# Kernel tuning notes

Hardware: AMD Instinct MI355X
Metric: run time of the kernel (lower is better)

## Reference

```python
import jax, jax.numpy as jnp
import numpy as np

N_NODES = 100000
N_EDGES = 640000
NODE_DIM = 128
EDGE_DIM = 128


def setup_inputs() -> dict:
    key = jax.random.key(0)
    ks = jax.random.split(key, 12)
    sc_n = 1.0 / np.sqrt(NODE_DIM).astype(np.float32)
    sc_e = 1.0 / np.sqrt(EDGE_DIM).astype(np.float32)
    sc_c = 1.0 / np.sqrt(2 * EDGE_DIM).astype(np.float32)
    return {
        "V": jax.random.normal(ks[0], (N_NODES, NODE_DIM), jnp.float32),
        "E": jax.random.normal(ks[1], (N_EDGES, EDGE_DIM), jnp.float32),
        "src": jax.random.randint(ks[2], (N_EDGES,), 0, N_NODES),
        "dst": jax.random.randint(ks[3], (N_EDGES,), 0, N_NODES),
        "U_w": jax.random.normal(ks[4], (EDGE_DIM, NODE_DIM), jnp.float32) * sc_n,
        "V_w": jax.random.normal(ks[5], (EDGE_DIM, NODE_DIM), jnp.float32) * sc_n,
        "P_w": jax.random.normal(ks[6], (EDGE_DIM, EDGE_DIM), jnp.float32) * sc_e,
        "P_b": jax.random.normal(ks[7], (EDGE_DIM,), jnp.float32) * sc_e,
        "W1": jax.random.normal(ks[8], (EDGE_DIM, 2 * EDGE_DIM), jnp.float32) * sc_c,
        "b1": jax.random.normal(ks[9], (EDGE_DIM,), jnp.float32) * sc_c,
        "W2": jax.random.normal(ks[10], (EDGE_DIM, EDGE_DIM), jnp.float32) * sc_e,
        "b2": jax.random.normal(ks[11], (EDGE_DIM,), jnp.float32) * sc_e,
    }


def reference(V, E, src, dst, U_w, V_w, P_w, P_b, W1, b1, W2, b2):
    # E = LeakyReLU(E)  (torch default negative_slope = 0.01)
    E_a = jax.nn.leaky_relu(E, negative_slope=0.01)  # [n_edges, edge_dim]
    # EdgePooling: P(tanh(U(V[src]) * V(V[dst])))
    h_src = jnp.einsum("en,dn->ed", V[src], U_w)      # gather + project
    h_dst = jnp.einsum("en,dn->ed", V[dst], V_w)
    pooled = jnp.tanh(h_src * h_dst) @ P_w.T + P_b    # [n_edges, edge_dim]
    # concat with edge data, then MLP (Linear+ReLU per layer)
    h = jnp.concatenate([pooled, E_a], axis=-1)       # [n_edges, 2*edge_dim]
    h = jax.nn.relu(h @ W1.T + b1)
    h = jax.nn.relu(h @ W2.T + b2)
    return h
```

## Files before the change

kernel.cpp:

```cpp
#include <hip/hip_runtime.h>

typedef __attribute__((ext_vector_type(8))) short short8;
typedef __attribute__((ext_vector_type(4))) short short4v;
typedef __attribute__((ext_vector_type(4))) float float4v;

#define N_EDGES 640000

__device__ __forceinline__ short f2bf(float f) {
  union { float f; unsigned u; } a; a.f = f;
  unsigned r = a.u + 0x7FFFu + ((a.u >> 16) & 1u);
  return (short)(r >> 16);
}

__device__ __forceinline__ float fast_tanh(float x) {
  float xc = fminf(fmaxf(x, -15.f), 15.f);
  float e = __expf(2.f * xc);
  return (e - 1.f) * __builtin_amdgcn_rcpf(e + 1.f);
}


__global__ void prep_cvt(const float* __restrict__ U_w, const float* __restrict__ V_w,
                         const float* __restrict__ W1, const float* __restrict__ W2,
                         short* __restrict__ ws) {
  int i = blockIdx.x * 256 + threadIdx.x;
  if (i < 16384) {
    ws[i] = f2bf(U_w[i]);
  } else if (i < 32768) {
    ws[i] = f2bf(V_w[i - 16384]);
  } else if (i < 49152) {
    int j = i - 32768;
    ws[i + 16384] = f2bf(W1[(j >> 7) * 256 + 128 + (j & 127)]);
  } else {
    int j = i - 49152;
    ws[i + 16384] = f2bf(W2[j]);
  }
}

__global__ void prep_mm(const float* __restrict__ W1, const float* __restrict__ P_w,
                        const float* __restrict__ P_b, const float* __restrict__ b1,
                        short* __restrict__ ws) {
  int i = blockIdx.x * 256 + threadIdx.x;
  int o = i >> 7, k = i & 127;
  const float* wrow = W1 + o * 256;
  const float* pcol = P_w + k;
  float a0 = 0.f, a1 = 0.f, a2 = 0.f, a3 = 0.f;
#pragma unroll
  for (int c = 0; c < 128; c += 4) {
    a0 += wrow[c]     * pcol[c * 128];
    a1 += wrow[c + 1] * pcol[(c + 1) * 128];
    a2 += wrow[c + 2] * pcol[(c + 2) * 128];
    a3 += wrow[c + 3] * pcol[(c + 3) * 128];
  }
  ws[32768 + i] = f2bf((a0 + a1) + (a2 + a3));
  if (i < 128) {
    const float* wr = W1 + i * 256;
    float b = b1[i];
    for (int c = 0; c < 128; c++) b += wr[c] * P_b[c];
    ((float*)(ws + 81920))[i] = b;
  }
}

__global__ __launch_bounds__(256, 4) void fused_kernel(
    const float* __restrict__ V, const float* __restrict__ E,
    const int* __restrict__ src, const int* __restrict__ dst,
    const short* __restrict__ wbf,
    const float* __restrict__ b2, float* __restrict__ out) {
  __shared__ short bufA[64][136];
  __shared__ short bufB[64][136];

  const int tid  = threadIdx.x;
  const int lane = tid & 63;
  const int wave = tid >> 6;
  const int l15  = lane & 15;
  const int quad = lane >> 4;
  const int eb   = blockIdx.x * 64;
  const int n0   = wave * 2;

  const short* wU   = wbf;
  const short* wV   = wbf + 16384;
  const short* wM1  = wbf + 32768;
  const short* wW1b = wbf + 49152;
  const short* wW2  = wbf + 65536;
  const float* b1p  = (const float*)(wbf + 81920);

  float b1v[2], b2v[2];
#pragma unroll
  for (int n = 0; n < 2; n++) {
    int c = (n0 + n) * 16 + l15;
    b1v[n] = b1p[c]; b2v[n] = b2[c];
  }

  for (int i = tid; i < 2048; i += 256) {
    int row = i >> 5;
    int ch  = i & 31;
    int e   = eb + row;
    int s = src[e], d = dst[e];
    float4v vs = *((const float4v*)(V + (size_t)s * 128) + ch);
    float4v vd = *((const float4v*)(V + (size_t)d * 128) + ch);
    short4v ps = {f2bf(vs[0]), f2bf(vs[1]), f2bf(vs[2]), f2bf(vs[3])};
    short4v pd = {f2bf(vd[0]), f2bf(vd[1]), f2bf(vd[2]), f2bf(vd[3])};
    *(short4v*)&bufA[row][ch * 4] = ps;
    *(short4v*)&bufB[row][ch * 4] = pd;
  }
  __syncthreads();

  short8 tpk[4];
  float4v ef[8];
#pragma unroll
  for (int m = 0; m < 4; m++) {
    float4v accS[2] = {(float4v){0.f,0.f,0.f,0.f}, (float4v){0.f,0.f,0.f,0.f}};
    float4v accD[2] = {(float4v){0.f,0.f,0.f,0.f}, (float4v){0.f,0.f,0.f,0.f}};
#pragma unroll
    for (int kk = 0; kk < 4; kk++) {
      short8 bU[2], bV[2];
#pragma unroll
      for (int n = 0; n < 2; n++) {
        const int off = ((n0 + n) * 16 + l15) * 128 + kk * 32 + quad * 8;
        bU[n] = *(const short8*)(wU + off);
        bV[n] = *(const short8*)(wV + off);
      }
      short8 aS = *(const short8*)&bufA[m * 16 + l15][kk * 32 + quad * 8];
      short8 aD = *(const short8*)&bufB[m * 16 + l15][kk * 32 + quad * 8];
#pragma unroll
      for (int n = 0; n < 2; n++) {
        accS[n] = __builtin_amdgcn_mfma_f32_16x16x32_bf16(aS, bU[n], accS[n], 0, 0, 0);
        accD[n] = __builtin_amdgcn_mfma_f32_16x16x32_bf16(aD, bV[n], accD[n], 0, 0, 0);
      }
    }
    if (m == 2) {
#pragma unroll
      for (int i = 0; i < 8; i++) {
        int idx = tid + (i << 8);
        int row = idx >> 5;
        int ch  = idx & 31;
        ef[i] = __builtin_nontemporal_load(
            (const float4v*)(E + (size_t)(eb + row) * 128) + ch);
      }
    }
    short tv[8];
#pragma unroll
    for (int n = 0; n < 2; n++)
#pragma unroll
      for (int r = 0; r < 4; r++)
        tv[n * 4 + r] = f2bf(fast_tanh(accS[n][r] * accD[n][r]));
    tpk[m] = (short8){tv[0], tv[1], tv[2], tv[3], tv[4], tv[5], tv[6], tv[7]};
  }
  __syncthreads();

#pragma unroll
  for (int m = 0; m < 4; m++)
#pragma unroll
    for (int n = 0; n < 2; n++)
#pragma unroll
      for (int r = 0; r < 4; r++)
        bufA[m * 16 + quad * 4 + r][(n0 + n) * 16 + l15] = tpk[m][n * 4 + r];
#pragma unroll
  for (int i = 0; i < 8; i++) {
    int idx = tid + (i << 8);
    int row = idx >> 5;
    int ch  = idx & 31;
    float4v x = ef[i];
    float e0 = x[0] > 0.f ? x[0] : 0.01f * x[0];
    float e1 = x[1] > 0.f ? x[1] : 0.01f * x[1];
    float e2 = x[2] > 0.f ? x[2] : 0.01f * x[2];
    float e3 = x[3] > 0.f ? x[3] : 0.01f * x[3];
    *(short4v*)&bufB[row][ch * 4] = (short4v){f2bf(e0), f2bf(e1), f2bf(e2), f2bf(e3)};
  }
  __syncthreads();

  float4v accH[4][2];
#pragma unroll
  for (int m = 0; m < 4; m++)
#pragma unroll
    for (int n = 0; n < 2; n++) accH[m][n] = (float4v){0.f, 0.f, 0.f, 0.f};
#pragma unroll
  for (int kk = 0; kk < 4; kk++) {
    short8 bM[2];
#pragma unroll
    for (int n = 0; n < 2; n++)
      bM[n] = *(const short8*)(wM1 + ((n0 + n) * 16 + l15) * 128 + kk * 32 + quad * 8);
#pragma unroll
    for (int m = 0; m < 4; m++) {
      short8 a = *(const short8*)&bufA[m * 16 + l15][kk * 32 + quad * 8];
#pragma unroll
      for (int n = 0; n < 2; n++)
        accH[m][n] = __builtin_amdgcn_mfma_f32_16x16x32_bf16(a, bM[n], accH[m][n], 0, 0, 0);
    }
  }
#pragma unroll
  for (int kk = 0; kk < 4; kk++) {
    short8 bW[2];
#pragma unroll
    for (int n = 0; n < 2; n++)
      bW[n] = *(const short8*)(wW1b + ((n0 + n) * 16 + l15) * 128 + kk * 32 + quad * 8);
#pragma unroll
    for (int m = 0; m < 4; m++) {
      short8 a = *(const short8*)&bufB[m * 16 + l15][kk * 32 + quad * 8];
#pragma unroll
      for (int n = 0; n < 2; n++)
        accH[m][n] = __builtin_amdgcn_mfma_f32_16x16x32_bf16(a, bW[n], accH[m][n], 0, 0, 0);
    }
  }
  __syncthreads();

#pragma unroll
  for (int m = 0; m < 4; m++)
#pragma unroll
    for (int n = 0; n < 2; n++)
#pragma unroll
      for (int r = 0; r < 4; r++) {
        float v = fmaxf(accH[m][n][r] + b1v[n], 0.f);
        bufA[m * 16 + quad * 4 + r][(n0 + n) * 16 + l15] = f2bf(v);
      }
  __syncthreads();

  {
    float4v accO[4][2];
#pragma unroll
    for (int m = 0; m < 4; m++)
#pragma unroll
      for (int n = 0; n < 2; n++) accO[m][n] = (float4v){0.f, 0.f, 0.f, 0.f};
#pragma unroll
    for (int kk = 0; kk < 4; kk++) {
      short8 bW[2];
#pragma unroll
      for (int n = 0; n < 2; n++)
        bW[n] = *(const short8*)(wW2 + ((n0 + n) * 16 + l15) * 128 + kk * 32 + quad * 8);
#pragma unroll
      for (int m = 0; m < 4; m++) {
        short8 a = *(const short8*)&bufA[m * 16 + l15][kk * 32 + quad * 8];
#pragma unroll
        for (int n = 0; n < 2; n++)
          accO[m][n] = __builtin_amdgcn_mfma_f32_16x16x32_bf16(a, bW[n], accO[m][n], 0, 0, 0);
      }
    }
#pragma unroll
    for (int m = 0; m < 4; m++)
#pragma unroll
      for (int n = 0; n < 2; n++)
#pragma unroll
        for (int r = 0; r < 4; r++) {
          float v = fmaxf(accO[m][n][r] + b2v[n], 0.f);
          __builtin_nontemporal_store(
              v, out + (size_t)(eb + m * 16 + quad * 4 + r) * 128 + (n0 + n) * 16 + l15);
        }
  }
}

extern "C" void kernel_launch(void* const* d_in, const int* in_sizes, int n_in,
                              void* d_out, int out_size, void* d_ws, size_t ws_size,
                              hipStream_t stream) {
  const float* V   = (const float*)d_in[0];
  const float* E   = (const float*)d_in[1];
  const int*   src = (const int*)d_in[2];
  const int*   dst = (const int*)d_in[3];
  const float* U_w = (const float*)d_in[4];
  const float* V_w = (const float*)d_in[5];
  const float* P_w = (const float*)d_in[6];
  const float* P_b = (const float*)d_in[7];
  const float* W1  = (const float*)d_in[8];
  const float* b1  = (const float*)d_in[9];
  const float* W2  = (const float*)d_in[10];
  const float* b2  = (const float*)d_in[11];
  short* ws = (short*)d_ws;

  hipLaunchKernelGGL(prep_cvt, dim3(256), dim3(256), 0, stream, U_w, V_w, W1, W2, ws);
  hipLaunchKernelGGL(prep_mm, dim3(64), dim3(256), 0, stream, W1, P_w, P_b, b1, ws);
  hipLaunchKernelGGL(fused_kernel, dim3(N_EDGES / 64), dim3(256), 0, stream,
                     V, E, src, dst, ws, b2, (float*)d_out);
}
```

Before: 775.0 us.

## Pre-convert V to bf16 and gather rows directly into swizzled LDS

Adds a prep kernel that converts the whole node feature table V to bf16 in workspace, so the per-edge gather reads half the bytes and uses global_load_lds to write straight into shared memory without register round-trips. LDS tiles drop their padding and use an XOR swizzle on 8-element chunks to avoid bank conflicts, and all reads and writes are updated to match. The E tile load moves up to overlap with the gather. In exchange there is an extra full pass over V (about 51MB read, 25MB written) each call, and the LDS swizzle adds index arithmetic.

```diff
diff --git a/kernel.cpp b/kernel.cpp
--- a/kernel.cpp
+++ b/kernel.cpp
@@ -5,6 +5,7 @@
 typedef __attribute__((ext_vector_type(4))) float float4v;
 
 #define N_EDGES 640000
+#define WS_VOFF 98304
 
 __device__ __forceinline__ short f2bf(float f) {
   union { float f; unsigned u; } a; a.f = f;
@@ -16,6 +17,12 @@
   float xc = fminf(fmaxf(x, -15.f), 15.f);
   float e = __expf(2.f * xc);
   return (e - 1.f) * __builtin_amdgcn_rcpf(e + 1.f);
+}
+
+__device__ __forceinline__ void gload_lds16(const short* g, short* l) {
+  __builtin_amdgcn_global_load_lds(
+      (const __attribute__((address_space(1))) unsigned int*)g,
+      (__attribute__((address_space(3))) unsigned int*)l, 16, 0, 0);
 }
 
 
@@ -60,13 +67,23 @@
   }
 }
 
+__global__ void prep_vbf(const float* __restrict__ V, short* __restrict__ ws) {
+  int i = blockIdx.x * 256 + threadIdx.x;
+  if (i >= 1600000) return;
+  const float4v* p = (const float4v*)V + (size_t)i * 2;
+  float4v a = p[0], b = p[1];
+  short8 o = {f2bf(a[0]), f2bf(a[1]), f2bf(a[2]), f2bf(a[3]),
+              f2bf(b[0]), f2bf(b[1]), f2bf(b[2]), f2bf(b[3])};
+  *(short8*)(ws + WS_VOFF + (size_t)i * 8) = o;
+}
+
 __global__ __launch_bounds__(256, 4) void fused_kernel(
-    const float* __restrict__ V, const float* __restrict__ E,
+    const float* __restrict__ E,
     const int* __restrict__ src, const int* __restrict__ dst,
     const short* __restrict__ wbf,
     const float* __restrict__ b2, float* __restrict__ out) {
-  __shared__ short bufA[64][136];
-  __shared__ short bufB[64][136];
+  __shared__ short bufA[64][128];
+  __shared__ short bufB[64][128];
 
   const int tid  = threadIdx.x;
   const int lane = tid & 63;
@@ -82,6 +99,7 @@
   const short* wW1b = wbf + 49152;
   const short* wW2  = wbf + 65536;
   const float* b1p  = (const float*)(wbf + 81920);
+  const short* Vbf  = wbf + WS_VOFF;
 
   float b1v[2], b2v[2];
 #pragma unroll
@@ -90,22 +108,35 @@
     b1v[n] = b1p[c]; b2v[n] = b2[c];
   }
 
-  for (int i = tid; i < 2048; i += 256) {
-    int row = i >> 5;
-    int ch  = i & 31;
-    int e   = eb + row;
-    int s = src[e], d = dst[e];
-    float4v vs = *((const float4v*)(V + (size_t)s * 128) + ch);
-    float4v vd = *((const float4v*)(V + (size_t)d * 128) + ch);
-    short4v ps = {f2bf(vs[0]), f2bf(vs[1]), f2bf(vs[2]), f2bf(vs[3])};
-    short4v pd = {f2bf(vd[0]), f2bf(vd[1]), f2bf(vd[2]), f2bf(vd[3])};
-    *(short4v*)&bufA[row][ch * 4] = ps;
-    *(short4v*)&bufB[row][ch * 4] = pd;
+  {
+    const int rb  = wave * 16;
+    const int sub = lane >> 4;
+    const int cs  = lane & 15;
+#pragma unroll
+    for (int i = 0; i < 4; i++) {
+      int row = rb + i * 4 + sub;
+      int e   = eb + row;
+      int si  = src[e];
+      int di  = dst[e];
+      int ch  = cs ^ (row & 7);
+      const short* gs = Vbf + (size_t)si * 128 + ch * 8;
+      const short* gd = Vbf + (size_t)di * 128 + ch * 8;
+      gload_lds16(gs, &bufA[rb + i * 4][0]);
+      gload_lds16(gd, &bufB[rb + i * 4][0]);
+    }
+  }
+  float4v ef[8];
+#pragma unroll
+  for (int i = 0; i < 8; i++) {
+    int idx = tid + (i << 8);
+    int row = idx >> 5;
+    int ch  = idx & 31;
+    ef[i] = __builtin_nontemporal_load(
+        (const float4v*)(E + (size_t)(eb + row) * 128) + ch);
   }
   __syncthreads();
 
   short8 tpk[4];
-  float4v ef[8];
 #pragma unroll
   for (int m = 0; m < 4; m++) {
     float4v accS[2] = {(float4v){0.f,0.f,0.f,0.f}, (float4v){0.f,0.f,0.f,0.f}};
@@ -119,24 +150,15 @@
         bU[n] = *(const short8*)(wU + off);
         bV[n] = *(const short8*)(wV + off);
       }
-      short8 aS = *(const short8*)&bufA[m * 16 + l15][kk * 32 + quad * 8];
-      short8 aD = *(const short8*)&bufB[m * 16 + l15][kk * 32 + quad * 8];
+      const int sw = ((kk * 4 + quad) ^ (l15 & 7)) * 8;
+      short8 aS = *(const short8*)&bufA[m * 16 + l15][sw];
+      short8 aD = *(const short8*)&bufB[m * 16 + l15][sw];
 #pragma unroll
       for (int n = 0; n < 2; n++) {
         accS[n] = __builtin_amdgcn_mfma_f32_16x16x32_bf16(aS, bU[n], accS[n], 0, 0, 0);
         accD[n] = __builtin_amdgcn_mfma_f32_16x16x32_bf16(aD, bV[n], accD[n], 0, 0, 0);
       }
     }
-    if (m == 2) {
-#pragma unroll
-      for (int i = 0; i < 8; i++) {
-        int idx = tid + (i << 8);
-        int row = idx >> 5;
-        int ch  = idx & 31;
-        ef[i] = __builtin_nontemporal_load(
-            (const float4v*)(E + (size_t)(eb + row) * 128) + ch);
-      }
-    }
     short tv[8];
 #pragma unroll
     for (int n = 0; n < 2; n++)
@@ -152,8 +174,11 @@
 #pragma unroll
     for (int n = 0; n < 2; n++)
 #pragma unroll
-      for (int r = 0; r < 4; r++)
-        bufA[m * 16 + quad * 4 + r][(n0 + n) * 16 + l15] = tpk[m][n * 4 + r];
+      for (int r = 0; r < 4; r++) {
+        int row = m * 16 + quad * 4 + r;
+        int col = (n0 + n) * 16 + l15;
+        bufA[row][((col >> 3) ^ (row & 7)) * 8 + (col & 7)] = tpk[m][n * 4 + r];
+      }
 #pragma unroll
   for (int i = 0; i < 8; i++) {
     int idx = tid + (i << 8);
@@ -164,7 +189,8 @@
     float e1 = x[1] > 0.f ? x[1] : 0.01f * x[1];
     float e2 = x[2] > 0.f ? x[2] : 0.01f * x[2];
     float e3 = x[3] > 0.f ? x[3] : 0.01f * x[3];
-    *(short4v*)&bufB[row][ch * 4] = (short4v){f2bf(e0), f2bf(e1), f2bf(e2), f2bf(e3)};
+    short4v pe = {f2bf(e0), f2bf(e1), f2bf(e2), f2bf(e3)};
+    *(short4v*)&bufB[row][((ch >> 1) ^ (row & 7)) * 8 + (ch & 1) * 4] = pe;
   }
   __syncthreads();
 
@@ -179,9 +205,10 @@
 #pragma unroll
     for (int n = 0; n < 2; n++)
       bM[n] = *(const short8*)(wM1 + ((n0 + n) * 16 + l15) * 128 + kk * 32 + quad * 8);
+    const int sw = ((kk * 4 + quad) ^ (l15 & 7)) * 8;
 #pragma unroll
     for (int m = 0; m < 4; m++) {
-      short8 a = *(const short8*)&bufA[m * 16 + l15][kk * 32 + quad * 8];
+      short8 a = *(const short8*)&bufA[m * 16 + l15][sw];
 #pragma unroll
       for (int n = 0; n < 2; n++)
         accH[m][n] = __builtin_amdgcn_mfma_f32_16x16x32_bf16(a, bM[n], accH[m][n], 0, 0, 0);
@@ -193,9 +220,10 @@
 #pragma unroll
     for (int n = 0; n < 2; n++)
       bW[n] = *(const short8*)(wW1b + ((n0 + n) * 16 + l15) * 128 + kk * 32 + quad * 8);
+    const int sw = ((kk * 4 + quad) ^ (l15 & 7)) * 8;
 #pragma unroll
     for (int m = 0; m < 4; m++) {
-      short8 a = *(const short8*)&bufB[m * 16 + l15][kk * 32 + quad * 8];
+      short8 a = *(const short8*)&bufB[m * 16 + l15][sw];
 #pragma unroll
       for (int n = 0; n < 2; n++)
         accH[m][n] = __builtin_amdgcn_mfma_f32_16x16x32_bf16(a, bW[n], accH[m][n], 0, 0, 0);
@@ -209,8 +237,10 @@
     for (int n = 0; n < 2; n++)
 #pragma unroll
       for (int r = 0; r < 4; r++) {
+        int row = m * 16 + quad * 4 + r;
+        int col = (n0 + n) * 16 + l15;
         float v = fmaxf(accH[m][n][r] + b1v[n], 0.f);
-        bufA[m * 16 + quad * 4 + r][(n0 + n) * 16 + l15] = f2bf(v);
+        bufA[row][((col >> 3) ^ (row & 7)) * 8 + (col & 7)] = f2bf(v);
       }
   __syncthreads();
 
@@ -226,9 +256,10 @@
 #pragma unroll
       for (int n = 0; n < 2; n++)
         bW[n] = *(const short8*)(wW2 + ((n0 + n) * 16 + l15) * 128 + kk * 32 + quad * 8);
+      const int sw = ((kk * 4 + quad) ^ (l15 & 7)) * 8;
 #pragma unroll
       for (int m = 0; m < 4; m++) {
-        short8 a = *(const short8*)&bufA[m * 16 + l15][kk * 32 + quad * 8];
+        short8 a = *(const short8*)&bufA[m * 16 + l15][sw];
 #pragma unroll
         for (int n = 0; n < 2; n++)
           accO[m][n] = __builtin_amdgcn_mfma_f32_16x16x32_bf16(a, bW[n], accO[m][n], 0, 0, 0);
@@ -266,6 +297,7 @@
 
   hipLaunchKernelGGL(prep_cvt, dim3(256), dim3(256), 0, stream, U_w, V_w, W1, W2, ws);
   hipLaunchKernelGGL(prep_mm, dim3(64), dim3(256), 0, stream, W1, P_w, P_b, b1, ws);
+  hipLaunchKernelGGL(prep_vbf, dim3(6250), dim3(256), 0, stream, V, ws);
   hipLaunchKernelGGL(fused_kernel, dim3(N_EDGES / 64), dim3(256), 0, stream,
-                     V, E, src, dst, ws, b2, (float*)d_out);
-}
+                     E, src, dst, ws, b2, (float*)d_out);
+}
```

Measured after the change: 859.4 us. +10.9%, slower.
